# Performance work log

Measured on AMD Instinct MI355X. Metric: run time of the kernel, lower is better.

## Reference

```python
import jax, jax.numpy as jnp
import numpy as np

N = 100000
E = 1600000
IN_C, HID_C, OUT_C = 128, 64, 40


def setup_inputs() -> dict:
    key = jax.random.key(0)
    ks = jax.random.split(key, 9)
    x = jax.random.normal(ks[0], (N, IN_C), dtype=jnp.float32)
    src = jax.random.randint(ks[1], (E,), 0, N, dtype=jnp.int64)
    dst = jax.random.randint(ks[2], (E,), 0, N, dtype=jnp.int64)
    edge_index = jnp.stack([src, dst], axis=0)
    def glorot(k, fan_in, fan_out):
        s = jnp.sqrt(6.0 / (fan_in + fan_out)).astype(jnp.float32)
        return jax.random.uniform(k, (fan_in, fan_out), jnp.float32, -s, s)
    return {
        "x": x,
        "edge_index": edge_index,
        "W1": glorot(ks[3], IN_C, HID_C), "b1": jnp.zeros((HID_C,), jnp.float32),
        "W2": glorot(ks[4], HID_C, HID_C), "b2": jnp.zeros((HID_C,), jnp.float32),
        "W3": glorot(ks[5], HID_C, OUT_C), "b3": jnp.zeros((OUT_C,), jnp.float32),
    }


def _gcn_norm(edge_index, n_nodes):
    # add self-loops, then symmetric normalization D^-1/2 (A+I) D^-1/2
    loops = jnp.arange(n_nodes, dtype=edge_index.dtype)
    src = jnp.concatenate([edge_index[0], loops])
    dst = jnp.concatenate([edge_index[1], loops])
    deg = jax.ops.segment_sum(jnp.ones_like(dst, dtype=jnp.float32), dst,
                              num_segments=n_nodes)
    dinv = jnp.where(deg > 0, jax.lax.rsqrt(deg), 0.0)
    norm = dinv[src] * dinv[dst]  # [E + N]
    return src, dst, norm


def _gcn_conv(h, W, b, src, dst, norm, n_nodes):
    h = h @ W                                   # [N, out]
    msg = norm[:, None] * h[src]                # gather + scale, [E+N, out]
    out = jax.ops.segment_sum(msg, dst, num_segments=n_nodes)  # scatter-add
    return out + b


def reference(x, edge_index, W1, b1, W2, b2, W3, b3):
    n_nodes = x.shape[0]
    src, dst, norm = _gcn_norm(edge_index, n_nodes)
    h = jax.nn.relu(_gcn_conv(x, W1, b1, src, dst, norm, n_nodes))
    # dropout(p=0.5) is identity in eval mode
    h = jax.nn.relu(_gcn_conv(h, W2, b2, src, dst, norm, n_nodes))
    out = _gcn_conv(h, W3, b3, src, dst, norm, n_nodes)
    return out
```

## Files before the change

kernel.cpp:

```cpp
#include <hip/hip_runtime.h>

#define N_NODES 100000
#define N_EDGES 1600000
#define NBUCK 196
#define BCAP 9600
#define CH 4096
#define NCHUNK ((N_EDGES + CH - 1) / CH)

typedef __attribute__((ext_vector_type(2))) _Float16 half2v;
typedef __attribute__((ext_vector_type(4))) _Float16 half4v;
typedef __attribute__((ext_vector_type(8))) _Float16 half8v;
typedef __attribute__((ext_vector_type(4))) float f32x4;

__device__ __forceinline__ float4 loadX4(const float* X, size_t idx) {
    return *(const float4*)(X + idx);
}
__device__ __forceinline__ float4 loadX4(const _Float16* X, size_t idx) {
    half4v h = *(const half4v*)(X + idx);
    return make_float4((float)h.x, (float)h.y, (float)h.z, (float)h.w);
}


__global__ __launch_bounds__(256) void zero_small(int* p, int n) {
    int i = blockIdx.x * blockDim.x + threadIdx.x;
    if (i < n) p[i] = 0;
}

__global__ __launch_bounds__(256) void multisplit(const int* __restrict__ src,
                                                  const int* __restrict__ dst,
                                                  int* cursor,
                                                  int* __restrict__ bucketed, int e) {
    __shared__ int cnt[NBUCK];
    __shared__ int basel[NBUCK];
    const int t = threadIdx.x;
    const int base_e = blockIdx.x * CH;

    int myS[16], myD[16];
    for (int i = t; i < NBUCK; i += 256) cnt[i] = 0;
    __syncthreads();

#pragma unroll
    for (int k = 0; k < 16; ++k) {
        int i = base_e + k * 256 + t;
        if (i < e) {
            myS[k] = src[i];
            myD[k] = dst[i];
            atomicAdd(&cnt[myD[k] >> 9], 1);
        } else {
            myD[k] = -1;
        }
    }
    __syncthreads();
    for (int i = t; i < NBUCK; i += 256) basel[i] = atomicAdd(&cursor[i], cnt[i]);
    __syncthreads();
    for (int i = t; i < NBUCK; i += 256) cnt[i] = 0;
    __syncthreads();

#pragma unroll
    for (int k = 0; k < 16; ++k) {
        if (myD[k] >= 0) {
            int b = myD[k] >> 9;
            int pos = basel[b] + atomicAdd(&cnt[b], 1);
            if (pos < BCAP)
                bucketed[(size_t)b * BCAP + pos] = ((myD[k] & 511) << 17) | myS[k];
        }
    }
}

__global__ __launch_bounds__(256) void bucket_scan(const int* __restrict__ cursor,
                                                   int* __restrict__ gbase) {
    __shared__ int sm[256];
    const int t = threadIdx.x;
    int v = (t < NBUCK) ? cursor[t] : 0;
    sm[t] = v;
    __syncthreads();
    for (int off = 1; off < 256; off <<= 1) {
        int u = (t >= off) ? sm[t - off] : 0;
        __syncthreads();
        sm[t] += u;
        __syncthreads();
    }
    if (t < NBUCK) gbase[t] = sm[t] - v;
    if (t == NBUCK - 1) gbase[NBUCK] = sm[t];
}

__global__ __launch_bounds__(512) void build_csr(const int* __restrict__ bucketed,
                                                 const int* __restrict__ gbase,
                                                 int* __restrict__ row_ptr,
                                                 float* __restrict__ dinv,
                                                 int* __restrict__ csr_src, int n) {
    __shared__ int vals[BCAP];
    __shared__ int cnt[512];
    __shared__ int lcur[512];
    const int b = blockIdx.x;
    const int t = threadIdx.x;
    const int nb0 = b * 512;
    const int nn = min(512, n - nb0);
    const int gb = gbase[b];
    const int m = gbase[b + 1] - gb;

    cnt[t] = 0;
    __syncthreads();
    for (int i = t; i < m; i += 512) {
        int v = bucketed[(size_t)b * BCAP + i];
        vals[i] = v;
        atomicAdd(&cnt[v >> 17], 1);
    }
    __syncthreads();

    int deg = cnt[t];
    for (int off = 1; off < 512; off <<= 1) {
        int u = (t >= off) ? cnt[t - off] : 0;
        __syncthreads();
        cnt[t] += u;
        __syncthreads();
    }
    int offv = cnt[t] - deg;
    __syncthreads();
    cnt[t] = offv;
    lcur[t] = 0;
    if (t < nn) {
        row_ptr[nb0 + t] = gb + offv;
        dinv[nb0 + t] = rsqrtf((float)(deg + 1));
    }
    if (b == NBUCK - 1 && t == 0) row_ptr[n] = gb + m;
    __syncthreads();

    for (int i = t; i < m; i += 512) {
        int v = vals[i];
        int node = v >> 17;
        int pos = atomicAdd(&lcur[node], 1);
        csr_src[gb + cnt[node] + pos] = v & 0x1FFFF;
    }
}


template <int K>
__global__ __launch_bounds__(256) void transpose_w(const float* __restrict__ W,
                                                   _Float16* __restrict__ Wt) {
    int i = blockIdx.x * 256 + threadIdx.x;
    if (i < K * 64) {
        int k = i >> 6, nn = i & 63;
        Wt[(size_t)nn * K + k] = (_Float16)W[i];
    }
}


__device__ __forceinline__ void stageX_rows(const float* X, _Float16* Xl, int t,
                                            int row0, int n, int K, int SP) {
    for (int i = t; i < 64 * K / 4; i += 256) {
        int r = i / (K / 4), c = (i % (K / 4)) * 4;
        int grow = min(row0 + r, n - 1);
        float4 v = *(const float4*)(X + (size_t)grow * K + c);
        half4v h = {(_Float16)v.x, (_Float16)v.y, (_Float16)v.z, (_Float16)v.w};
        *(half4v*)(Xl + r * SP + c) = h;
    }
}
__device__ __forceinline__ void stageX_rows(const _Float16* X, _Float16* Xl, int t,
                                            int row0, int n, int K, int SP) {
    for (int i = t; i < 64 * K / 8; i += 256) {
        int r = i / (K / 8), c = (i % (K / 8)) * 8;
        int grow = min(row0 + r, n - 1);
        *(half8v*)(Xl + r * SP + c) = *(const half8v*)(X + (size_t)grow * K + c);
    }
}

template <int K, typename XT>
__global__ __launch_bounds__(256) void gemm_mfma64(const XT* __restrict__ X,
                                                   const _Float16* __restrict__ Wt,
                                                   const float* __restrict__ dinv,
                                                   _Float16* __restrict__ Y, int n) {
    constexpr int SP = K + 8;
    __shared__ _Float16 Xl[64 * SP];
    __shared__ _Float16 Wl[64 * SP];
    const int t = threadIdx.x;
    const int wave = t >> 6, lane = t & 63;
    const int row0 = blockIdx.x * 64;
    const int m = lane & 15, quad = lane >> 4;

    for (int i = t; i < 64 * K / 8; i += 256) {
        int r = i / (K / 8), c = (i % (K / 8)) * 8;
        *(half8v*)(Wl + r * SP + c) = *(const half8v*)(Wt + (size_t)r * K + c);
    }
    stageX_rows(X, Xl, t, row0, n, K, SP);
    __syncthreads();

    f32x4 acc[4] = {{0,0,0,0},{0,0,0,0},{0,0,0,0},{0,0,0,0}};
#pragma unroll
    for (int k0 = 0; k0 < K; k0 += 32) {
        half8v a = *(const half8v*)(Xl + (wave * 16 + m) * SP + k0 + quad * 8);
#pragma unroll
        for (int ct = 0; ct < 4; ++ct) {
            half8v b = *(const half8v*)(Wl + (ct * 16 + m) * SP + k0 + quad * 8);
            acc[ct] = __builtin_amdgcn_mfma_f32_16x16x32_f16(a, b, acc[ct], 0, 0, 0);
        }
    }

    float dv[4];
#pragma unroll
    for (int r = 0; r < 4; ++r) {
        int row = row0 + wave * 16 + quad * 4 + r;
        dv[r] = dinv[min(row, n - 1)];
    }
#pragma unroll
    for (int ct = 0; ct < 4; ++ct) {
#pragma unroll
        for (int r = 0; r < 4; ++r) {
            int row = row0 + wave * 16 + quad * 4 + r;
            if (row < n)
                Y[(size_t)row * 64 + ct * 16 + m] = (_Float16)(dv[r] * acc[ct][r]);
        }
    }
}


template <int K, int COUT, typename XT>
__global__ __launch_bounds__(256) void gemm_rt(const XT* __restrict__ X,
                                               const float* __restrict__ W,
                                               const float* __restrict__ dinv,
                                               _Float16* __restrict__ Y, int n) {
    constexpr int KC = 64;
    constexpr int S = KC + 4;
    constexpr int NCH = K / KC;
    __shared__ float Xl[64 * S];
    __shared__ float Wl[KC * COUT];

    const int t = threadIdx.x;
    const int row0 = blockIdx.x * 64;
    const int cg = (t & 15) * 4;
    const int rg = (t >> 4) * 4;

    float acc[4][4] = {};

#pragma unroll
    for (int ch = 0; ch < NCH; ++ch) {
        const int k0 = ch * KC;
        for (int i = t; i < 64 * KC / 4; i += 256) {
            int r = i >> 4;
            int k = (i & 15) * 4;
            int grow = min(row0 + r, n - 1);
            *(float4*)(Xl + r * S + k) = loadX4(X, (size_t)grow * K + k0 + k);
        }
        for (int i = t; i < KC * COUT / 4; i += 256) {
            *(float4*)(Wl + i * 4) = *(const float4*)(W + (size_t)k0 * COUT + (size_t)i * 4);
        }
        __syncthreads();

        if (cg < COUT) {
#pragma unroll 4
            for (int k = 0; k < KC; ++k) {
                float4 w = *(const float4*)(Wl + k * COUT + cg);
                float x0 = Xl[(rg + 0) * S + k];
                float x1 = Xl[(rg + 1) * S + k];
                float x2 = Xl[(rg + 2) * S + k];
                float x3 = Xl[(rg + 3) * S + k];
                acc[0][0] += x0 * w.x; acc[0][1] += x0 * w.y; acc[0][2] += x0 * w.z; acc[0][3] += x0 * w.w;
                acc[1][0] += x1 * w.x; acc[1][1] += x1 * w.y; acc[1][2] += x1 * w.z; acc[1][3] += x1 * w.w;
                acc[2][0] += x2 * w.x; acc[2][1] += x2 * w.y; acc[2][2] += x2 * w.z; acc[2][3] += x2 * w.w;
                acc[3][0] += x3 * w.x; acc[3][1] += x3 * w.y; acc[3][2] += x3 * w.z; acc[3][3] += x3 * w.w;
            }
        }
        __syncthreads();
    }

    if (cg < COUT) {
#pragma unroll
        for (int r = 0; r < 4; ++r) {
            int row = row0 + rg + r;
            if (row < n) {
                float d = dinv[row];
                half4v o = { (_Float16)(d * acc[r][0]), (_Float16)(d * acc[r][1]),
                             (_Float16)(d * acc[r][2]), (_Float16)(d * acc[r][3]) };
                *(half4v*)(Y + (size_t)row * COUT + cg) = o;
            }
        }
    }
}


template <bool RELU>
__global__ __launch_bounds__(256) void aggregate64f(const _Float16* __restrict__ tS,
                                                    const int* __restrict__ row_ptr,
                                                    const int* __restrict__ csr_src,
                                                    const float* __restrict__ dinv,
                                                    const float* __restrict__ bias,
                                                    _Float16* __restrict__ out, int n) {
    const int t = threadIdx.x;
    const int lane = t & 63;
    const int c8 = lane & 7;
    const int node = blockIdx.x * 32 + (t >> 3);
    const half8v* tS8 = (const half8v*)tS;
    const int bpb = (lane & 56) << 2;

    const int beg = row_ptr[node];
    const int cnt = row_ptr[node + 1] - beg;
    const int cl = (cnt > 0) ? cnt - 1 : 0;

    int mc = cnt;
    mc = max(mc, __shfl_xor(mc, 8));
    mc = max(mc, __shfl_xor(mc, 16));
    mc = max(mc, __shfl_xor(mc, 32));

    half8v acc0, acc1;
#pragma unroll
    for (int i = 0; i < 8; ++i) { acc0[i] = (_Float16)0; acc1[i] = (_Float16)0; }

    for (int j0 = 0; j0 < mc; j0 += 8) {
        int sj = csr_src[beg + min(j0 + c8, cl)];
#pragma unroll
        for (int jj = 0; jj < 8; ++jj) {
            int e = __builtin_amdgcn_ds_bpermute(bpb + jj * 4, sj);
            if (j0 + jj < cnt) {
                half8v v = tS8[(size_t)e * 8 + c8];
                if (jj & 1) acc1 += v; else acc0 += v;
            }
        }
    }

    float acc[8];
#pragma unroll
    for (int i = 0; i < 8; ++i) acc[i] = (float)acc0[i] + (float)acc1[i];

    half8v selfh = tS8[(size_t)node * 8 + c8];
    float4 b0 = ((const float4*)bias)[c8 * 2];
    float4 b1 = ((const float4*)bias)[c8 * 2 + 1];
    const float bb[8] = {b0.x, b0.y, b0.z, b0.w, b1.x, b1.y, b1.z, b1.w};
    float d = dinv[node];
    half8v o;
#pragma unroll
    for (int i = 0; i < 8; ++i) {
        float v = bb[i] + d * (acc[i] + (float)selfh[i]);
        if (RELU) v = fmaxf(v, 0.0f);
        o[i] = (_Float16)v;
    }
    ((half8v*)out)[(size_t)node * 8 + c8] = o;
}


__global__ __launch_bounds__(256) void aggregate40z(const _Float16* __restrict__ tS,
                                                    const int* __restrict__ row_ptr,
                                                    const int* __restrict__ csr_src,
                                                    const float* __restrict__ dinv,
                                                    const float* __restrict__ bias,
                                                    float* __restrict__ out, int n) {
    const int t = threadIdx.x;
    const int lane = t & 63;
    const int wave = t >> 6;
    const int g = lane / 10;
    const int c10 = lane - g * 10;
    const int node = blockIdx.x * 24 + wave * 6 + g;
    const bool act = (g < 6) && (node < n);
    const half4v* tS4 = (const half4v*)tS;
    const int bpb = g * 40;

    const int nclamp = act ? node : 0;
    const int beg = row_ptr[nclamp];
    const int cnt = act ? (row_ptr[nclamp + 1] - beg) : 0;
    const int cl = (cnt > 0) ? cnt - 1 : 0;

    int mc = cnt;
    mc = max(mc, __shfl_xor(mc, 1));
    mc = max(mc, __shfl_xor(mc, 2));
    mc = max(mc, __shfl_xor(mc, 4));
    mc = max(mc, __shfl_xor(mc, 8));
    mc = max(mc, __shfl_xor(mc, 16));
    mc = max(mc, __shfl_xor(mc, 32));

    half4v a0, a1;
#pragma unroll
    for (int i = 0; i < 4; ++i) { a0[i] = (_Float16)0; a1[i] = (_Float16)0; }

    for (int j0 = 0; j0 < mc; j0 += 10) {
        int sj = csr_src[beg + min(j0 + c10, cl)];
#pragma unroll
        for (int jj = 0; jj < 10; ++jj) {
            int e = __builtin_amdgcn_ds_bpermute(bpb + jj * 4, sj);
            if (j0 + jj < cnt) {
                half4v v = tS4[(size_t)e * 10 + c10];
                if (jj & 1) a1 += v; else a0 += v;
            }
        }
    }

    if (act) {
        float acc[4];
#pragma unroll
        for (int i = 0; i < 4; ++i) acc[i] = (float)a0[i] + (float)a1[i];

        half4v selfh = tS4[(size_t)node * 10 + c10];
        float4 b = ((const float4*)bias)[c10];
        float d = dinv[node];
        float4 o;
        o.x = b.x + d * (acc[0] + (float)selfh[0]);
        o.y = b.y + d * (acc[1] + (float)selfh[1]);
        o.z = b.z + d * (acc[2] + (float)selfh[2]);
        o.w = b.w + d * (acc[3] + (float)selfh[3]);
        *(float4*)(out + (size_t)node * 40 + c10 * 4) = o;
    }
}


extern "C" void kernel_launch(void* const* d_in, const int* in_sizes, int n_in,
                              void* d_out, int out_size, void* d_ws, size_t ws_size,
                              hipStream_t stream) {
    const float* x  = (const float*)d_in[0];
    const int*   ei = (const int*)d_in[1];
    const int*   src = ei;
    const int*   dst = ei + N_EDGES;
    const float* W1 = (const float*)d_in[2];
    const float* b1 = (const float*)d_in[3];
    const float* W2 = (const float*)d_in[4];
    const float* b2 = (const float*)d_in[5];
    const float* W3 = (const float*)d_in[6];
    const float* b3 = (const float*)d_in[7];
    float* out = (float*)d_out;

    const int N = N_NODES, E = N_EDGES;

    char* p = (char*)d_ws;
    int*   cursor   = (int*)p;              p += 256 * 4;
    int*   gbase    = (int*)p;              p += 256 * 4;
    float* dinv     = (float*)p;            p += (size_t)N * 4;
    int*   row_ptr  = (int*)p;              p += (size_t)(N + 4) * 4;
    int*   bucketed = (int*)p;              p += (size_t)NBUCK * BCAP * 4;
    int*   csr_src  = (int*)p;              p += (size_t)(E + 64) * 4;
    p = (char*)(((size_t)p + 15) & ~(size_t)15);
    _Float16* Wt1   = (_Float16*)p;         p += (size_t)64 * 128 * 2;
    _Float16* Wt2   = (_Float16*)p;         p += (size_t)64 * 64 * 2;
    _Float16* bufA  = (_Float16*)p;         p += (size_t)(N + 64) * 64 * 2;
    p = (char*)(((size_t)p + 15) & ~(size_t)15);
    _Float16* bufB  = (_Float16*)p;         p += (size_t)N * 64 * 2;

    zero_small<<<1, 256, 0, stream>>>(cursor, NBUCK);
    transpose_w<128><<<32, 256, 0, stream>>>(W1, Wt1);
    transpose_w<64><<<16, 256, 0, stream>>>(W2, Wt2);
    multisplit<<<NCHUNK, 256, 0, stream>>>(src, dst, cursor, bucketed, E);
    bucket_scan<<<1, 256, 0, stream>>>(cursor, gbase);
    build_csr<<<NBUCK, 512, 0, stream>>>(bucketed, gbase, row_ptr, dinv, csr_src, N);

    const int agg64Grid = N / 32;
    const int agg40Grid = (N + 23) / 24;
    const int gemmGrid = (N + 63) / 64;

    gemm_mfma64<128, float><<<gemmGrid, 256, 0, stream>>>(x, Wt1, dinv, bufA, N);
    aggregate64f<true><<<agg64Grid, 256, 0, stream>>>(bufA, row_ptr, csr_src, dinv, b1, bufB, N);

    gemm_mfma64<64, _Float16><<<gemmGrid, 256, 0, stream>>>(bufB, Wt2, dinv, bufA, N);
    aggregate64f<true><<<agg64Grid, 256, 0, stream>>>(bufA, row_ptr, csr_src, dinv, b2, bufB, N);

    gemm_rt<64, 40, _Float16><<<gemmGrid, 256, 0, stream>>>(bufB, W3, dinv, bufA, N);
    aggregate40z<<<agg40Grid, 256, 0, stream>>>(bufA, row_ptr, csr_src, dinv, b3, out, N);
}
```

Measured before the change: 329.8 us.

## Sort nodes by degree for balanced aggregation and use zero-row padding

Builds a degree histogram and counting-sort permutation so aggregation groups sharing a wave process nodes of similar degree, cutting divergence from the per-wave max-degree loop. Out-of-range neighbor slots now read a zeroed padding row at index n instead of branching. The 40-channel aggregate switches to 8-half loads with 5 lanes per node and 12 nodes per wave. It adds three small kernels and scattered writes to output rows, since consecutive groups no longer map to consecutive nodes.

```diff
diff --git a/kernel.cpp b/kernel.cpp
--- a/kernel.cpp
+++ b/kernel.cpp
@@ -6,6 +6,7 @@
 #define BCAP 9600
 #define CH 4096
 #define NCHUNK ((N_EDGES + CH - 1) / CH)
+#define DBINS 64
 
 typedef __attribute__((ext_vector_type(2))) _Float16 half2v;
 typedef __attribute__((ext_vector_type(4))) _Float16 half4v;
@@ -135,6 +136,45 @@
 }
 
 
+__global__ __launch_bounds__(256) void deg_hist(const int* __restrict__ row_ptr,
+                                                int* __restrict__ hist, int n) {
+    int i = blockIdx.x * 256 + threadIdx.x;
+    if (i < n) {
+        int deg = row_ptr[i + 1] - row_ptr[i];
+        atomicAdd(&hist[min(deg, DBINS - 1)], 1);
+    }
+}
+
+__global__ __launch_bounds__(64) void hist_scan(const int* __restrict__ hist,
+                                                int* __restrict__ base) {
+    __shared__ int sm[DBINS];
+    const int t = threadIdx.x;
+    int v = hist[t];
+    sm[t] = v;
+    __syncthreads();
+    for (int off = 1; off < DBINS; off <<= 1) {
+        int u = (t >= off) ? sm[t - off] : 0;
+        __syncthreads();
+        sm[t] += u;
+        __syncthreads();
+    }
+    base[t] = sm[t] - v;
+}
+
+__global__ __launch_bounds__(256) void perm_scatter(const int* __restrict__ row_ptr,
+                                                    const int* __restrict__ base,
+                                                    int* cursor,
+                                                    int* __restrict__ perm, int n) {
+    int i = blockIdx.x * 256 + threadIdx.x;
+    if (i < n) {
+        int deg = row_ptr[i + 1] - row_ptr[i];
+        int b = min(deg, DBINS - 1);
+        int pos = base[b] + atomicAdd(&cursor[b], 1);
+        perm[pos] = i;
+    }
+}
+
+
 template <int K>
 __global__ __launch_bounds__(256) void transpose_w(const float* __restrict__ W,
                                                    _Float16* __restrict__ Wt) {
@@ -177,6 +217,8 @@
     const int wave = t >> 6, lane = t & 63;
     const int row0 = blockIdx.x * 64;
     const int m = lane & 15, quad = lane >> 4;
+
+    if (blockIdx.x == 0 && t < 32) ((int*)(Y + (size_t)n * 64))[t] = 0;
 
     for (int i = t; i < 64 * K / 8; i += 256) {
         int r = i / (K / 8), c = (i % (K / 8)) * 8;
@@ -229,6 +271,8 @@
     const int row0 = blockIdx.x * 64;
     const int cg = (t & 15) * 4;
     const int rg = (t >> 4) * 4;
+
+    if (blockIdx.x == 0 && t < COUT / 2) ((int*)(Y + (size_t)n * COUT))[t] = 0;
 
     float acc[4][4] = {};
 
@@ -279,16 +323,17 @@
 
 
 template <bool RELU>
-__global__ __launch_bounds__(256) void aggregate64f(const _Float16* __restrict__ tS,
+__global__ __launch_bounds__(256) void aggregate64g(const _Float16* __restrict__ tS,
                                                     const int* __restrict__ row_ptr,
                                                     const int* __restrict__ csr_src,
+                                                    const int* __restrict__ perm,
                                                     const float* __restrict__ dinv,
                                                     const float* __restrict__ bias,
                                                     _Float16* __restrict__ out, int n) {
     const int t = threadIdx.x;
     const int lane = t & 63;
     const int c8 = lane & 7;
-    const int node = blockIdx.x * 32 + (t >> 3);
+    const int node = perm[blockIdx.x * 32 + (t >> 3)];
     const half8v* tS8 = (const half8v*)tS;
     const int bpb = (lane & 56) << 2;
 
@@ -310,10 +355,9 @@
 #pragma unroll
         for (int jj = 0; jj < 8; ++jj) {
             int e = __builtin_amdgcn_ds_bpermute(bpb + jj * 4, sj);
-            if (j0 + jj < cnt) {
-                half8v v = tS8[(size_t)e * 8 + c8];
-                if (jj & 1) acc1 += v; else acc0 += v;
-            }
+            e = (j0 + jj < cnt) ? e : n;
+            half8v v = tS8[(size_t)e * 8 + c8];
+            if (jj & 1) acc1 += v; else acc0 += v;
         }
     }
 
@@ -337,25 +381,26 @@
 }
 
 
-__global__ __launch_bounds__(256) void aggregate40z(const _Float16* __restrict__ tS,
+__global__ __launch_bounds__(256) void aggregate40p(const _Float16* __restrict__ tS,
                                                     const int* __restrict__ row_ptr,
                                                     const int* __restrict__ csr_src,
+                                                    const int* __restrict__ perm,
                                                     const float* __restrict__ dinv,
                                                     const float* __restrict__ bias,
                                                     float* __restrict__ out, int n) {
     const int t = threadIdx.x;
     const int lane = t & 63;
     const int wave = t >> 6;
-    const int g = lane / 10;
-    const int c10 = lane - g * 10;
-    const int node = blockIdx.x * 24 + wave * 6 + g;
-    const bool act = (g < 6) && (node < n);
-    const half4v* tS4 = (const half4v*)tS;
-    const int bpb = g * 40;
-
-    const int nclamp = act ? node : 0;
-    const int beg = row_ptr[nclamp];
-    const int cnt = act ? (row_ptr[nclamp + 1] - beg) : 0;
+    const int g = lane / 5;
+    const int c5 = lane - g * 5;
+    const int gi = blockIdx.x * 48 + wave * 12 + g;
+    const bool act = (g < 12) && (gi < n);
+    const int node = act ? perm[gi] : 0;
+    const half8v* tS8r = (const half8v*)tS;
+    const int bpb = g * 20;
+
+    const int beg = act ? row_ptr[node] : 0;
+    const int cnt = act ? (row_ptr[node + 1] - beg) : 0;
     const int cl = (cnt > 0) ? cnt - 1 : 0;
 
     int mc = cnt;
@@ -366,36 +411,41 @@
     mc = max(mc, __shfl_xor(mc, 16));
     mc = max(mc, __shfl_xor(mc, 32));
 
-    half4v a0, a1;
-#pragma unroll
-    for (int i = 0; i < 4; ++i) { a0[i] = (_Float16)0; a1[i] = (_Float16)0; }
-
-    for (int j0 = 0; j0 < mc; j0 += 10) {
-        int sj = csr_src[beg + min(j0 + c10, cl)];
-#pragma unroll
-        for (int jj = 0; jj < 10; ++jj) {
+    half8v a0, a1;
+#pragma unroll
+    for (int i = 0; i < 8; ++i) { a0[i] = (_Float16)0; a1[i] = (_Float16)0; }
+
+    for (int j0 = 0; j0 < mc; j0 += 5) {
+        int sj = csr_src[beg + min(j0 + c5, cl)];
+#pragma unroll
+        for (int jj = 0; jj < 5; ++jj) {
             int e = __builtin_amdgcn_ds_bpermute(bpb + jj * 4, sj);
-            if (j0 + jj < cnt) {
-                half4v v = tS4[(size_t)e * 10 + c10];
-                if (jj & 1) a1 += v; else a0 += v;
-            }
+            e = (j0 + jj < cnt) ? e : n;
+            half8v v = tS8r[(size_t)e * 5 + c5];
+            if (jj & 1) a1 += v; else a0 += v;
         }
     }
 
     if (act) {
-        float acc[4];
-#pragma unroll
-        for (int i = 0; i < 4; ++i) acc[i] = (float)a0[i] + (float)a1[i];
-
-        half4v selfh = tS4[(size_t)node * 10 + c10];
-        float4 b = ((const float4*)bias)[c10];
+        float acc[8];
+#pragma unroll
+        for (int i = 0; i < 8; ++i) acc[i] = (float)a0[i] + (float)a1[i];
+
+        half8v selfh = tS8r[(size_t)node * 5 + c5];
+        float4 b0 = ((const float4*)bias)[c5 * 2];
+        float4 b1 = ((const float4*)bias)[c5 * 2 + 1];
         float d = dinv[node];
-        float4 o;
-        o.x = b.x + d * (acc[0] + (float)selfh[0]);
-        o.y = b.y + d * (acc[1] + (float)selfh[1]);
-        o.z = b.z + d * (acc[2] + (float)selfh[2]);
-        o.w = b.w + d * (acc[3] + (float)selfh[3]);
-        *(float4*)(out + (size_t)node * 40 + c10 * 4) = o;
+        float4 o0, o1;
+        o0.x = b0.x + d * (acc[0] + (float)selfh[0]);
+        o0.y = b0.y + d * (acc[1] + (float)selfh[1]);
+        o0.z = b0.z + d * (acc[2] + (float)selfh[2]);
+        o0.w = b0.w + d * (acc[3] + (float)selfh[3]);
+        o1.x = b1.x + d * (acc[4] + (float)selfh[4]);
+        o1.y = b1.y + d * (acc[5] + (float)selfh[5]);
+        o1.z = b1.z + d * (acc[6] + (float)selfh[6]);
+        o1.w = b1.w + d * (acc[7] + (float)selfh[7]);
+        *(float4*)(out + (size_t)node * 40 + c5 * 8) = o0;
+        *(float4*)(out + (size_t)node * 40 + c5 * 8 + 4) = o1;
     }
 }
 
@@ -420,8 +470,10 @@
     char* p = (char*)d_ws;
     int*   cursor   = (int*)p;              p += 256 * 4;
     int*   gbase    = (int*)p;              p += 256 * 4;
+    int*   histx    = (int*)p;              p += 256 * 4;
     float* dinv     = (float*)p;            p += (size_t)N * 4;
     int*   row_ptr  = (int*)p;              p += (size_t)(N + 4) * 4;
+    int*   perm     = (int*)p;              p += (size_t)N * 4;
     int*   bucketed = (int*)p;              p += (size_t)NBUCK * BCAP * 4;
     int*   csr_src  = (int*)p;              p += (size_t)(E + 64) * 4;
     p = (char*)(((size_t)p + 15) & ~(size_t)15);
@@ -431,23 +483,33 @@
     p = (char*)(((size_t)p + 15) & ~(size_t)15);
     _Float16* bufB  = (_Float16*)p;         p += (size_t)N * 64 * 2;
 
+    int* hist    = histx;
+    int* cursor2 = histx + 64;
+    int* dbase   = histx + 128;
+
     zero_small<<<1, 256, 0, stream>>>(cursor, NBUCK);
+    zero_small<<<1, 256, 0, stream>>>(histx, 128);
     transpose_w<128><<<32, 256, 0, stream>>>(W1, Wt1);
     transpose_w<64><<<16, 256, 0, stream>>>(W2, Wt2);
     multisplit<<<NCHUNK, 256, 0, stream>>>(src, dst, cursor, bucketed, E);
     bucket_scan<<<1, 256, 0, stream>>>(cursor, gbase);
     build_csr<<<NBUCK, 512, 0, stream>>>(bucketed, gbase, row_ptr, dinv, csr_src, N);
 
+    const int nThreadGrid = (N + 255) / 256;
+    deg_hist<<<nThreadGrid, 256, 0, stream>>>(row_ptr, hist, N);
+    hist_scan<<<1, 64, 0, stream>>>(hist, dbase);
+    perm_scatter<<<nThreadGrid, 256, 0, stream>>>(row_ptr, dbase, cursor2, perm, N);
+
     const int agg64Grid = N / 32;
-    const int agg40Grid = (N + 23) / 24;
+    const int agg40Grid = (N + 47) / 48;
     const int gemmGrid = (N + 63) / 64;
 
     gemm_mfma64<128, float><<<gemmGrid, 256, 0, stream>>>(x, Wt1, dinv, bufA, N);
-    aggregate64f<true><<<agg64Grid, 256, 0, stream>>>(bufA, row_ptr, csr_src, dinv, b1, bufB, N);
+    aggregate64g<true><<<agg64Grid, 256, 0, stream>>>(bufA, row_ptr, csr_src, perm, dinv, b1, bufB, N);
 
     gemm_mfma64<64, _Float16><<<gemmGrid, 256, 0, stream>>>(bufB, Wt2, dinv, bufA, N);
-    aggregate64f<true><<<agg64Grid, 256, 0, stream>>>(bufA, row_ptr, csr_src, dinv, b2, bufB, N);
+    aggregate64g<true><<<agg64Grid, 256, 0, stream>>>(bufA, row_ptr, csr_src, perm, dinv, b2, bufB, N);
 
     gemm_rt<64, 40, _Float16><<<gemmGrid, 256, 0, stream>>>(bufB, W3, dinv, bufA, N);
-    aggregate40z<<<agg40Grid, 256, 0, stream>>>(bufA, row_ptr, csr_src, dinv, b3, out, N);
-}
+    aggregate40p<<<agg40Grid, 256, 0, stream>>>(bufA, row_ptr, csr_src, perm, dinv, b3, out, N);
+}
```

After: 865.5 us. 162% more time.
